# Kernel optimization log

Measured on AMD Instinct MI355X. Metric: run time of the kernel, lower is better.

The kernel has to match this reference:

```python
import jax, jax.numpy as jnp
import numpy as np
import math

D_MODEL, Q, V, H = 512, 64, 64, 8
NEG = float(-2**32 + 1)


def setup_inputs() -> dict:
    key = jax.random.key(0)
    ks = jax.random.split(key, 10)
    B, S = 16, 1024
    x = jax.random.normal(ks[0], (B, S, D_MODEL), dtype=jnp.float32)
    padding_mask = jax.random.randint(ks[1], (B, S), 0, 2, dtype=jnp.int32)
    s = 0.02
    wq = jax.random.normal(ks[2], (D_MODEL, Q * H), dtype=jnp.float32) * s
    bq = jnp.zeros((Q * H,), jnp.float32)
    wk = jax.random.normal(ks[3], (D_MODEL, Q * H), dtype=jnp.float32) * s
    bk = jnp.zeros((Q * H,), jnp.float32)
    wv = jax.random.normal(ks[4], (D_MODEL, V * H), dtype=jnp.float32) * s
    bv = jnp.zeros((V * H,), jnp.float32)
    wo = jax.random.normal(ks[5], (V * H, D_MODEL), dtype=jnp.float32) * s
    bo = jnp.zeros((D_MODEL,), jnp.float32)
    return {"x": x, "padding_mask": padding_mask, "wq": wq, "bq": bq,
            "wk": wk, "bk": bk, "wv": wv, "bv": bv, "wo": wo, "bo": bo}


def _heads_major(t, h, d):
    # torch: cat(t.chunk(h, dim=-1), dim=0): (B,S,h*d) -> (h*B,S,d), head-major
    B, S, _ = t.shape
    return t.reshape(B, S, h, d).transpose(2, 0, 1, 3).reshape(h * B, S, d)


def reference(x, padding_mask, wq, bq, wk, bk, wv, bv, wo, bo):
    B, S, _ = x.shape
    Qh = _heads_major(x @ wq + bq, H, Q)          # (h*B, S, Q)
    Kh = _heads_major(x @ wk + bk, H, Q)          # (h*B, S, Q)
    Vh = _heads_major(x @ wv + bv, H, V)          # (h*B, S, V)
    score = jnp.einsum('nsq,ntq->nst', Qh, Kh) / math.sqrt(Q)  # (h*B,S,S)
    raw_score = score
    # padding mask flattened BATCH-major (B*h), applied to HEAD-major score
    # -- this index mismatch is faithful to the original torch code.
    pm = jnp.broadcast_to(padding_mask[:, None, None, :], (B, H, S, S))
    pm = pm.reshape(B * H, S, S)
    score = jnp.where(pm == 0, NEG, score)
    attn = jnp.einsum('nst,ntv->nsv', jax.nn.softmax(score, axis=-1), Vh)
    # torch: cat(attn.chunk(h, dim=0), dim=-1): (h*B,S,V) -> (B,S,h*V)
    heads = attn.reshape(H, B, S, V).transpose(1, 2, 0, 3).reshape(B, S, H * V)
    out = heads @ wo + bo                          # (B, S, d_model)
    return out, raw_score
```

## Files before the change

kernel.cpp:

```cpp
#include <hip/hip_runtime.h>
#include <hip/hip_bf16.h>

typedef __attribute__((ext_vector_type(8))) short short8;
typedef __attribute__((ext_vector_type(4))) short short4v;
typedef __attribute__((ext_vector_type(4))) float floatx4;

#define NEGVAL (-4294967296.0f)

__device__ __forceinline__ short f2bf(float f) {
    union { float f; unsigned u; } v; v.f = f;
    unsigned r = v.u + 0x7fffu + ((v.u >> 16) & 1u);
    return (short)(r >> 16);
}

__global__ __launch_bounds__(256) void qkv_kernel(
    const float* __restrict__ x,
    const float* __restrict__ wq, const float* __restrict__ bq,
    const float* __restrict__ wk, const float* __restrict__ bk,
    const float* __restrict__ wv, const float* __restrict__ bv,
    short* __restrict__ qws, short* __restrict__ kws, short* __restrict__ vws)
{
    __shared__ __align__(16) short lA[128 * 72];
    __shared__ __align__(16) short lB[128 * 72];

    const int tid  = threadIdx.x;
    const int wave = tid >> 6, lane = tid & 63;
    const int g = lane >> 4, l16 = lane & 15;
    const int m0 = blockIdx.x * 128;
    const int c0 = blockIdx.y * 128;
    const int wsel = c0 >> 9;
    const int cmat = c0 & 511;
    const float* W    = (wsel == 0) ? wq : (wsel == 1) ? wk : wv;
    const float* bias = (wsel == 0) ? bq : (wsel == 1) ? bk : bv;
    short* dst        = (wsel == 0) ? qws : (wsel == 1) ? kws : vws;

    floatx4 acc[4][4];
    #pragma unroll
    for (int i = 0; i < 4; i++)
        #pragma unroll
        for (int j = 0; j < 4; j++) acc[i][j] = (floatx4){0.f, 0.f, 0.f, 0.f};

    const int wm = (wave & 1) * 64, wn = (wave >> 1) * 64;

    for (int k0 = 0; k0 < 512; k0 += 32) {
        #pragma unroll
        for (int it = 0; it < 4; ++it) {
            int u = tid + (it << 8);
            int row = u >> 3, cs = (u & 7) * 4;
            const float4 a = *(const float4*)&x[(size_t)(m0 + row) * 512 + k0 + cs];
            short4v s4;
            s4[0] = f2bf(a.x); s4[1] = f2bf(a.y); s4[2] = f2bf(a.z); s4[3] = f2bf(a.w);
            *(short4v*)&lA[row * 72 + cs] = s4;
        }
        #pragma unroll
        for (int it = 0; it < 4; ++it) {
            int u = tid + (it << 8);
            int d = u >> 5, cs = (u & 31) * 4;
            const float4 b = *(const float4*)&W[(size_t)(k0 + d) * 512 + cmat + cs];
            lB[(cs + 0) * 72 + d] = f2bf(b.x);
            lB[(cs + 1) * 72 + d] = f2bf(b.y);
            lB[(cs + 2) * 72 + d] = f2bf(b.z);
            lB[(cs + 3) * 72 + d] = f2bf(b.w);
        }
        __syncthreads();

        short8 af[4], bf[4];
        #pragma unroll
        for (int i = 0; i < 4; i++)
            af[i] = *(short8*)&lA[(wm + i * 16 + l16) * 72 + (g << 3)];
        #pragma unroll
        for (int j = 0; j < 4; j++)
            bf[j] = *(short8*)&lB[(wn + j * 16 + l16) * 72 + (g << 3)];
        #pragma unroll
        for (int i = 0; i < 4; i++)
            #pragma unroll
            for (int j = 0; j < 4; j++)
                acc[i][j] = __builtin_amdgcn_mfma_f32_16x16x32_bf16(af[i], bf[j], acc[i][j], 0, 0, 0);
        __syncthreads();
    }

    #pragma unroll
    for (int j = 0; j < 4; j++) {
        int cb = cmat + wn + j * 16 + l16;
        float bv_ = bias[cb];
        int h = cb >> 6, qd = cb & 63;
        #pragma unroll
        for (int i = 0; i < 4; i++) {
            #pragma unroll
            for (int r = 0; r < 4; r++) {
                int m = m0 + wm + i * 16 + (g << 2) + r;
                int b = m >> 10, s = m & 1023;
                float v = acc[i][j][r] + bv_;
                dst[(((size_t)((h << 4) + b) << 10) + s) * 64 + qd] = f2bf(v);
            }
        }
    }
}

__global__ __launch_bounds__(256) void attn_kernel(
    const short* __restrict__ qws, const short* __restrict__ kws,
    const short* __restrict__ vws, const int* __restrict__ pm,
    float* __restrict__ raw, short* __restrict__ attnws)
{
    __shared__ __align__(16) short lK[64 * 72];
    __shared__ __align__(16) short lVt[64 * 72];
    __shared__ __align__(16) short lP[4][16 * 72];
    __shared__ float lMask[1024];

    const int tid  = threadIdx.x;
    const int wave = tid >> 6, lane = tid & 63;
    const int g = lane >> 4, l16 = lane & 15;
    const int bx = blockIdx.x;
    const int n  = blockIdx.y;
    const int mb = n >> 3;

    for (int i = tid; i < 1024; i += 256) lMask[i] = (float)pm[(mb << 10) + i];

    const int srow = (bx << 6) + (wave << 4) + l16;
    const size_t qbase = (((size_t)n << 10) + srow) * 64;
    short8 qf0 = *(const short8*)&qws[qbase + (g << 3)];
    short8 qf1 = *(const short8*)&qws[qbase + 32 + (g << 3)];

    float m_r[4], l_r[4];
    floatx4 Of[4];
    #pragma unroll
    for (int r = 0; r < 4; r++) { m_r[r] = -INFINITY; l_r[r] = 0.f; }
    #pragma unroll
    for (int v = 0; v < 4; v++) Of[v] = (floatx4){0.f, 0.f, 0.f, 0.f};

    float* rawn = raw + ((size_t)n << 20);
    const int rowbase = (bx << 6) + (wave << 4) + (g << 2);

    for (int c = 0; c < 16; ++c) {
        const int tc = c << 6;
        #pragma unroll
        for (int it = 0; it < 2; ++it) {
            int u = tid + (it << 8);
            int trow = u >> 3, seg = (u & 7) << 3;
            const size_t gaddr = (((size_t)n << 10) + tc + trow) * 64 + seg;
            *(uint4*)&lK[trow * 72 + seg] = *(const uint4*)&kws[gaddr];
            union { uint4 u4; short s8[8]; } vv;
            vv.u4 = *(const uint4*)&vws[gaddr];
            #pragma unroll
            for (int j = 0; j < 8; j++) lVt[(seg + j) * 72 + trow] = vv.s8[j];
        }
        __syncthreads();

        floatx4 sc[4];
        #pragma unroll
        for (int nt = 0; nt < 4; ++nt) {
            floatx4 a = (floatx4){0.f, 0.f, 0.f, 0.f};
            short8 b0 = *(short8*)&lK[(nt * 16 + l16) * 72 + (g << 3)];
            short8 b1 = *(short8*)&lK[(nt * 16 + l16) * 72 + 32 + (g << 3)];
            a = __builtin_amdgcn_mfma_f32_16x16x32_bf16(qf0, b0, a, 0, 0, 0);
            a = __builtin_amdgcn_mfma_f32_16x16x32_bf16(qf1, b1, a, 0, 0, 0);
            sc[nt] = a;
        }

        float p[4][4];
        float cmax[4] = {-INFINITY, -INFINITY, -INFINITY, -INFINITY};
        #pragma unroll
        for (int nt = 0; nt < 4; ++nt) {
            int col = tc + nt * 16 + l16;
            float mk = lMask[col];
            #pragma unroll
            for (int r = 0; r < 4; r++) {
                float v = sc[nt][r] * 0.125f;
                __builtin_nontemporal_store(v, &rawn[((size_t)(rowbase + r) << 10) + col]);
                float mv = (mk != 0.f) ? v : NEGVAL;
                p[nt][r] = mv;
                cmax[r] = fmaxf(cmax[r], mv);
            }
        }
        #pragma unroll
        for (int off = 1; off < 16; off <<= 1) {
            #pragma unroll
            for (int r = 0; r < 4; r++) cmax[r] = fmaxf(cmax[r], __shfl_xor(cmax[r], off));
        }
        float alpha[4], rs[4];
        #pragma unroll
        for (int r = 0; r < 4; r++) {
            float mn = fmaxf(m_r[r], cmax[r]);
            alpha[r] = __expf(m_r[r] - mn);
            m_r[r] = mn;
            rs[r] = 0.f;
        }
        #pragma unroll
        for (int nt = 0; nt < 4; ++nt) {
            #pragma unroll
            for (int r = 0; r < 4; r++) {
                float e = __expf(p[nt][r] - m_r[r]);
                p[nt][r] = e;
                rs[r] += e;
            }
        }
        #pragma unroll
        for (int off = 1; off < 16; off <<= 1) {
            #pragma unroll
            for (int r = 0; r < 4; r++) rs[r] += __shfl_xor(rs[r], off);
        }
        #pragma unroll
        for (int r = 0; r < 4; r++) l_r[r] = l_r[r] * alpha[r] + rs[r];
        #pragma unroll
        for (int v = 0; v < 4; v++)
            #pragma unroll
            for (int r = 0; r < 4; r++) Of[v][r] *= alpha[r];

        #pragma unroll
        for (int nt = 0; nt < 4; ++nt)
            #pragma unroll
            for (int r = 0; r < 4; r++)
                lP[wave][((g << 2) + r) * 72 + nt * 16 + l16] = f2bf(p[nt][r]);
        __syncthreads();

        #pragma unroll
        for (int ks = 0; ks < 2; ++ks) {
            short8 pa = *(short8*)&lP[wave][l16 * 72 + ks * 32 + (g << 3)];
            #pragma unroll
            for (int v = 0; v < 4; v++) {
                short8 vb = *(short8*)&lVt[(v * 16 + l16) * 72 + ks * 32 + (g << 3)];
                Of[v] = __builtin_amdgcn_mfma_f32_16x16x32_bf16(pa, vb, Of[v], 0, 0, 0);
            }
        }
        __syncthreads();
    }

    const int h = n >> 4, b = n & 15;
    #pragma unroll
    for (int r = 0; r < 4; r++) {
        int s = (bx << 6) + (wave << 4) + (g << 2) + r;
        float inv = 1.f / l_r[r];
        size_t base = ((size_t)((b << 10) + s)) * 512 + (h << 6);
        #pragma unroll
        for (int v = 0; v < 4; v++)
            attnws[base + v * 16 + l16] = f2bf(Of[v][r] * inv);
    }
}

__global__ __launch_bounds__(256) void outproj_kernel(
    const short* __restrict__ attnws, const float* __restrict__ wo,
    const float* __restrict__ bo, float* __restrict__ out)
{
    __shared__ __align__(16) short lA[128 * 72];
    __shared__ __align__(16) short lB[128 * 72];

    const int tid  = threadIdx.x;
    const int wave = tid >> 6, lane = tid & 63;
    const int g = lane >> 4, l16 = lane & 15;
    const int m0 = blockIdx.x * 128;
    const int c0 = blockIdx.y * 128;

    floatx4 acc[4][4];
    #pragma unroll
    for (int i = 0; i < 4; i++)
        #pragma unroll
        for (int j = 0; j < 4; j++) acc[i][j] = (floatx4){0.f, 0.f, 0.f, 0.f};

    const int wm = (wave & 1) * 64, wn = (wave >> 1) * 64;

    for (int k0 = 0; k0 < 512; k0 += 32) {
        #pragma unroll
        for (int it = 0; it < 2; ++it) {
            int u = tid + (it << 8);
            int row = u >> 2, seg = (u & 3) << 3;
            *(uint4*)&lA[row * 72 + seg] =
                *(const uint4*)&attnws[(size_t)(m0 + row) * 512 + k0 + seg];
        }
        #pragma unroll
        for (int it = 0; it < 4; ++it) {
            int u = tid + (it << 8);
            int d = u >> 5, cs = (u & 31) * 4;
            const float4 b = *(const float4*)&wo[(size_t)(k0 + d) * 512 + c0 + cs];
            lB[(cs + 0) * 72 + d] = f2bf(b.x);
            lB[(cs + 1) * 72 + d] = f2bf(b.y);
            lB[(cs + 2) * 72 + d] = f2bf(b.z);
            lB[(cs + 3) * 72 + d] = f2bf(b.w);
        }
        __syncthreads();

        short8 af[4], bf[4];
        #pragma unroll
        for (int i = 0; i < 4; i++)
            af[i] = *(short8*)&lA[(wm + i * 16 + l16) * 72 + (g << 3)];
        #pragma unroll
        for (int j = 0; j < 4; j++)
            bf[j] = *(short8*)&lB[(wn + j * 16 + l16) * 72 + (g << 3)];
        #pragma unroll
        for (int i = 0; i < 4; i++)
            #pragma unroll
            for (int j = 0; j < 4; j++)
                acc[i][j] = __builtin_amdgcn_mfma_f32_16x16x32_bf16(af[i], bf[j], acc[i][j], 0, 0, 0);
        __syncthreads();
    }

    #pragma unroll
    for (int j = 0; j < 4; j++) {
        int cg = c0 + wn + j * 16 + l16;
        float bb = bo[cg];
        #pragma unroll
        for (int i = 0; i < 4; i++) {
            #pragma unroll
            for (int r = 0; r < 4; r++) {
                int m = m0 + wm + i * 16 + (g << 2) + r;
                out[(size_t)m * 512 + cg] = acc[i][j][r] + bb;
            }
        }
    }
}

extern "C" void kernel_launch(void* const* d_in, const int* in_sizes, int n_in,
                              void* d_out, int out_size, void* d_ws, size_t ws_size,
                              hipStream_t stream) {
    const float* x  = (const float*)d_in[0];
    const int*   pm = (const int*)d_in[1];
    const float* wq = (const float*)d_in[2];
    const float* bq = (const float*)d_in[3];
    const float* wk = (const float*)d_in[4];
    const float* bk = (const float*)d_in[5];
    const float* wv = (const float*)d_in[6];
    const float* bv = (const float*)d_in[7];
    const float* wo = (const float*)d_in[8];
    const float* bo = (const float*)d_in[9];

    float* out = (float*)d_out;
    float* raw = out + (size_t)16 * 1024 * 512;

    short* qws    = (short*)d_ws;
    short* kws    = qws + (size_t)128 * 1024 * 64;
    short* vws    = kws + (size_t)128 * 1024 * 64;
    short* attnws = vws + (size_t)128 * 1024 * 64;

    qkv_kernel<<<dim3(128, 12), 256, 0, stream>>>(x, wq, bq, wk, bk, wv, bv, qws, kws, vws);
    attn_kernel<<<dim3(16, 128), 256, 0, stream>>>(qws, kws, vws, pm, raw, attnws);
    outproj_kernel<<<dim3(128, 4), 256, 0, stream>>>(attnws, wo, bo, out);
}
```

Baseline: 817.9 us.

## Pre-convert inputs to bf16, stage tiles via global_load_lds with XOR swizzle, transpose V

Adds separate kernels that convert x to bf16 and convert plus transpose the weight matrices to bf16, so the GEMM kernels no longer convert in the inner loop. The GEMM and attention tile loads now go directly from global memory to LDS through global_load_lds, using an XOR-swizzled layout in place of padding. The QKV kernel writes V already transposed, so the attention kernel no longer transposes it through LDS, and one barrier before the PV step is removed. The cost is two extra kernel launches and extra workspace traffic. The workspace is reused, with x stored in the attention-output buffer, which depends on launch order.

```diff
diff --git a/kernel.cpp b/kernel.cpp
--- a/kernel.cpp
+++ b/kernel.cpp
@@ -13,15 +13,66 @@
     return (short)(r >> 16);
 }
 
+__device__ __forceinline__ void load_lds16(const void* g, void* l) {
+    __builtin_amdgcn_global_load_lds(
+        (const __attribute__((address_space(1))) unsigned int*)g,
+        (__attribute__((address_space(3))) unsigned int*)l, 16, 0, 0);
+}
+
+__global__ __launch_bounds__(256) void convx_kernel(
+    const float* __restrict__ x, short* __restrict__ xbf)
+{
+    size_t i = ((size_t)blockIdx.x * 256 + threadIdx.x) << 3;
+    float4 a = *(const float4*)&x[i];
+    float4 b = *(const float4*)&x[i + 4];
+    short8 s;
+    s[0] = f2bf(a.x); s[1] = f2bf(a.y); s[2] = f2bf(a.z); s[3] = f2bf(a.w);
+    s[4] = f2bf(b.x); s[5] = f2bf(b.y); s[6] = f2bf(b.z); s[7] = f2bf(b.w);
+    *(short8*)&xbf[i] = s;
+}
+
+__global__ __launch_bounds__(256) void convw_kernel(
+    const float* __restrict__ wq, const float* __restrict__ wk,
+    const float* __restrict__ wv, const float* __restrict__ wo,
+    short* __restrict__ wt, short* __restrict__ wot)
+{
+    __shared__ __align__(16) short t[64 * 72];
+    const int tid  = threadIdx.x;
+    const int mat  = blockIdx.x >> 6;
+    const int tile = blockIdx.x & 63;
+    const int tn = (tile >> 3) << 6, tk = (tile & 7) << 6;
+    const float* W = (mat == 0) ? wq : (mat == 1) ? wk : (mat == 2) ? wv : wo;
+    short* dst = (mat < 3) ? (wt + ((size_t)mat << 18)) : wot;
+
+    #pragma unroll
+    for (int it = 0; it < 4; ++it) {
+        int u = tid + (it << 8);
+        int kr = u >> 4, c4 = (u & 15) << 2;
+        const float4 a = *(const float4*)&W[(size_t)(tk + kr) * 512 + tn + c4];
+        short4v s;
+        s[0] = f2bf(a.x); s[1] = f2bf(a.y); s[2] = f2bf(a.z); s[3] = f2bf(a.w);
+        *(short4v*)&t[kr * 72 + c4] = s;
+    }
+    __syncthreads();
+    #pragma unroll
+    for (int it = 0; it < 2; ++it) {
+        int u = tid + (it << 8);
+        int nr = u >> 3, kc = (u & 7) << 3;
+        short8 s;
+        #pragma unroll
+        for (int j = 0; j < 8; ++j) s[j] = t[(kc + j) * 72 + nr];
+        *(short8*)&dst[(size_t)(tn + nr) * 512 + tk + kc] = s;
+    }
+}
+
 __global__ __launch_bounds__(256) void qkv_kernel(
-    const float* __restrict__ x,
-    const float* __restrict__ wq, const float* __restrict__ bq,
-    const float* __restrict__ wk, const float* __restrict__ bk,
-    const float* __restrict__ wv, const float* __restrict__ bv,
+    const short* __restrict__ xbf, const short* __restrict__ wt,
+    const float* __restrict__ bq, const float* __restrict__ bk,
+    const float* __restrict__ bv,
     short* __restrict__ qws, short* __restrict__ kws, short* __restrict__ vws)
 {
-    __shared__ __align__(16) short lA[128 * 72];
-    __shared__ __align__(16) short lB[128 * 72];
+    __shared__ __align__(16) short lA[128 * 32];
+    __shared__ __align__(16) short lB[128 * 32];
 
     const int tid  = threadIdx.x;
     const int wave = tid >> 6, lane = tid & 63;
@@ -30,9 +81,7 @@
     const int c0 = blockIdx.y * 128;
     const int wsel = c0 >> 9;
     const int cmat = c0 & 511;
-    const float* W    = (wsel == 0) ? wq : (wsel == 1) ? wk : wv;
     const float* bias = (wsel == 0) ? bq : (wsel == 1) ? bk : bv;
-    short* dst        = (wsel == 0) ? qws : (wsel == 1) ? kws : vws;
 
     floatx4 acc[4][4];
     #pragma unroll
@@ -41,57 +90,75 @@
         for (int j = 0; j < 4; j++) acc[i][j] = (floatx4){0.f, 0.f, 0.f, 0.f};
 
     const int wm = (wave & 1) * 64, wn = (wave >> 1) * 64;
+    const int lrow = lane >> 2, lch = lane & 3;
+    const int stg = wave << 5;
 
     for (int k0 = 0; k0 < 512; k0 += 32) {
         #pragma unroll
-        for (int it = 0; it < 4; ++it) {
-            int u = tid + (it << 8);
-            int row = u >> 3, cs = (u & 7) * 4;
-            const float4 a = *(const float4*)&x[(size_t)(m0 + row) * 512 + k0 + cs];
-            short4v s4;
-            s4[0] = f2bf(a.x); s4[1] = f2bf(a.y); s4[2] = f2bf(a.z); s4[3] = f2bf(a.w);
-            *(short4v*)&lA[row * 72 + cs] = s4;
-        }
-        #pragma unroll
-        for (int it = 0; it < 4; ++it) {
-            int u = tid + (it << 8);
-            int d = u >> 5, cs = (u & 31) * 4;
-            const float4 b = *(const float4*)&W[(size_t)(k0 + d) * 512 + cmat + cs];
-            lB[(cs + 0) * 72 + d] = f2bf(b.x);
-            lB[(cs + 1) * 72 + d] = f2bf(b.y);
-            lB[(cs + 2) * 72 + d] = f2bf(b.z);
-            lB[(cs + 3) * 72 + d] = f2bf(b.w);
-        }
-        __syncthreads();
-
-        short8 af[4], bf[4];
+        for (int i = 0; i < 2; ++i) {
+            int r = stg + (i << 4) + lrow;
+            load_lds16(&xbf[(size_t)(m0 + r) * 512 + k0 + ((lch ^ ((r >> 1) & 3)) << 3)],
+                       &lA[(stg + (i << 4)) * 32]);
+        }
+        #pragma unroll
+        for (int i = 0; i < 2; ++i) {
+            int r = stg + (i << 4) + lrow;
+            load_lds16(&wt[((size_t)wsel << 18) + (size_t)(cmat + r) * 512 + k0 +
+                           ((lch ^ ((r >> 1) & 3)) << 3)],
+                       &lB[(stg + (i << 4)) * 32]);
+        }
+        __syncthreads();
+
+        short8 af[4], bfr[4];
+        #pragma unroll
+        for (int i = 0; i < 4; i++) {
+            int row = wm + i * 16 + l16;
+            af[i] = *(short8*)&lA[row * 32 + (((g << 3)) ^ ((((row) >> 1) & 3) << 3))];
+        }
+        #pragma unroll
+        for (int j = 0; j < 4; j++) {
+            int row = wn + j * 16 + l16;
+            bfr[j] = *(short8*)&lB[row * 32 + (((g << 3)) ^ ((((row) >> 1) & 3) << 3))];
+        }
         #pragma unroll
         for (int i = 0; i < 4; i++)
-            af[i] = *(short8*)&lA[(wm + i * 16 + l16) * 72 + (g << 3)];
-        #pragma unroll
-        for (int j = 0; j < 4; j++)
-            bf[j] = *(short8*)&lB[(wn + j * 16 + l16) * 72 + (g << 3)];
-        #pragma unroll
-        for (int i = 0; i < 4; i++)
             #pragma unroll
             for (int j = 0; j < 4; j++)
-                acc[i][j] = __builtin_amdgcn_mfma_f32_16x16x32_bf16(af[i], bf[j], acc[i][j], 0, 0, 0);
-        __syncthreads();
-    }
-
-    #pragma unroll
-    for (int j = 0; j < 4; j++) {
-        int cb = cmat + wn + j * 16 + l16;
-        float bv_ = bias[cb];
-        int h = cb >> 6, qd = cb & 63;
-        #pragma unroll
-        for (int i = 0; i < 4; i++) {
-            #pragma unroll
-            for (int r = 0; r < 4; r++) {
-                int m = m0 + wm + i * 16 + (g << 2) + r;
+                acc[i][j] = __builtin_amdgcn_mfma_f32_16x16x32_bf16(af[i], bfr[j], acc[i][j], 0, 0, 0);
+        __syncthreads();
+    }
+
+    if (wsel < 2) {
+        short* dst = wsel ? kws : qws;
+        #pragma unroll
+        for (int j = 0; j < 4; j++) {
+            int cb = cmat + wn + j * 16 + l16;
+            float bv_ = bias[cb];
+            int h = cb >> 6, qd = cb & 63;
+            #pragma unroll
+            for (int i = 0; i < 4; i++) {
+                #pragma unroll
+                for (int r = 0; r < 4; r++) {
+                    int m = m0 + wm + i * 16 + (g << 2) + r;
+                    int b = m >> 10, s = m & 1023;
+                    dst[(((size_t)((h << 4) + b) << 10) + s) * 64 + qd] = f2bf(acc[i][j][r] + bv_);
+                }
+            }
+        }
+    } else {
+        #pragma unroll
+        for (int j = 0; j < 4; j++) {
+            int cb = cmat + wn + j * 16 + l16;
+            float bv_ = bias[cb];
+            int h = cb >> 6, qd = cb & 63;
+            #pragma unroll
+            for (int i = 0; i < 4; i++) {
+                int m = m0 + wm + i * 16 + (g << 2);
                 int b = m >> 10, s = m & 1023;
-                float v = acc[i][j][r] + bv_;
-                dst[(((size_t)((h << 4) + b) << 10) + s) * 64 + qd] = f2bf(v);
+                short4v sv;
+                #pragma unroll
+                for (int r = 0; r < 4; r++) sv[r] = f2bf(acc[i][j][r] + bv_);
+                *(short4v*)&vws[(((size_t)((h << 4) + b) << 6) + qd) * 1024 + s] = sv;
             }
         }
     }
@@ -102,8 +169,8 @@
     const short* __restrict__ vws, const int* __restrict__ pm,
     float* __restrict__ raw, short* __restrict__ attnws)
 {
-    __shared__ __align__(16) short lK[64 * 72];
-    __shared__ __align__(16) short lVt[64 * 72];
+    __shared__ __align__(16) short lK[64 * 64];
+    __shared__ __align__(16) short lVt[64 * 64];
     __shared__ __align__(16) short lP[4][16 * 72];
     __shared__ float lMask[1024];
 
@@ -130,28 +197,33 @@
 
     float* rawn = raw + ((size_t)n << 20);
     const int rowbase = (bx << 6) + (wave << 4) + (g << 2);
+    const int lrow = lane >> 3, lch = lane & 7;
+    const int stg = wave << 4;
 
     for (int c = 0; c < 16; ++c) {
         const int tc = c << 6;
         #pragma unroll
-        for (int it = 0; it < 2; ++it) {
-            int u = tid + (it << 8);
-            int trow = u >> 3, seg = (u & 7) << 3;
-            const size_t gaddr = (((size_t)n << 10) + tc + trow) * 64 + seg;
-            *(uint4*)&lK[trow * 72 + seg] = *(const uint4*)&kws[gaddr];
-            union { uint4 u4; short s8[8]; } vv;
-            vv.u4 = *(const uint4*)&vws[gaddr];
-            #pragma unroll
-            for (int j = 0; j < 8; j++) lVt[(seg + j) * 72 + trow] = vv.s8[j];
+        for (int i = 0; i < 2; ++i) {
+            int r = stg + (i << 3) + lrow;
+            load_lds16(&kws[(((size_t)n << 10) + tc + r) * 64 + ((lch ^ (r & 7)) << 3)],
+                       &lK[(stg + (i << 3)) * 64]);
+        }
+        #pragma unroll
+        for (int i = 0; i < 2; ++i) {
+            int r = stg + (i << 3) + lrow;
+            load_lds16(&vws[(((size_t)n << 6) + r) * 1024 + tc + ((lch ^ (r & 7)) << 3)],
+                       &lVt[(stg + (i << 3)) * 64]);
         }
         __syncthreads();
 
         floatx4 sc[4];
         #pragma unroll
         for (int nt = 0; nt < 4; ++nt) {
+            int rr = nt * 16 + l16;
+            int sw = (rr & 7) << 3;
             floatx4 a = (floatx4){0.f, 0.f, 0.f, 0.f};
-            short8 b0 = *(short8*)&lK[(nt * 16 + l16) * 72 + (g << 3)];
-            short8 b1 = *(short8*)&lK[(nt * 16 + l16) * 72 + 32 + (g << 3)];
+            short8 b0 = *(short8*)&lK[rr * 64 + ((g << 3) ^ sw)];
+            short8 b1 = *(short8*)&lK[rr * 64 + ((32 + (g << 3)) ^ sw)];
             a = __builtin_amdgcn_mfma_f32_16x16x32_bf16(qf0, b0, a, 0, 0, 0);
             a = __builtin_amdgcn_mfma_f32_16x16x32_bf16(qf1, b1, a, 0, 0, 0);
             sc[nt] = a;
@@ -211,14 +283,14 @@
             #pragma unroll
             for (int r = 0; r < 4; r++)
                 lP[wave][((g << 2) + r) * 72 + nt * 16 + l16] = f2bf(p[nt][r]);
-        __syncthreads();
 
         #pragma unroll
         for (int ks = 0; ks < 2; ++ks) {
             short8 pa = *(short8*)&lP[wave][l16 * 72 + ks * 32 + (g << 3)];
             #pragma unroll
             for (int v = 0; v < 4; v++) {
-                short8 vb = *(short8*)&lVt[(v * 16 + l16) * 72 + ks * 32 + (g << 3)];
+                int vr = v * 16 + l16;
+                short8 vb = *(short8*)&lVt[vr * 64 + ((ks * 32 + (g << 3)) ^ ((vr & 7) << 3))];
                 Of[v] = __builtin_amdgcn_mfma_f32_16x16x32_bf16(pa, vb, Of[v], 0, 0, 0);
             }
         }
@@ -238,11 +310,11 @@
 }
 
 __global__ __launch_bounds__(256) void outproj_kernel(
-    const short* __restrict__ attnws, const float* __restrict__ wo,
+    const short* __restrict__ attnws, const short* __restrict__ wot,
     const float* __restrict__ bo, float* __restrict__ out)
 {
-    __shared__ __align__(16) short lA[128 * 72];
-    __shared__ __align__(16) short lB[128 * 72];
+    __shared__ __align__(16) short lA[128 * 32];
+    __shared__ __align__(16) short lB[128 * 32];
 
     const int tid  = threadIdx.x;
     const int wave = tid >> 6, lane = tid & 63;
@@ -257,39 +329,40 @@
         for (int j = 0; j < 4; j++) acc[i][j] = (floatx4){0.f, 0.f, 0.f, 0.f};
 
     const int wm = (wave & 1) * 64, wn = (wave >> 1) * 64;
+    const int lrow = lane >> 2, lch = lane & 3;
+    const int stg = wave << 5;
 
     for (int k0 = 0; k0 < 512; k0 += 32) {
         #pragma unroll
-        for (int it = 0; it < 2; ++it) {
-            int u = tid + (it << 8);
-            int row = u >> 2, seg = (u & 3) << 3;
-            *(uint4*)&lA[row * 72 + seg] =
-                *(const uint4*)&attnws[(size_t)(m0 + row) * 512 + k0 + seg];
-        }
-        #pragma unroll
-        for (int it = 0; it < 4; ++it) {
-            int u = tid + (it << 8);
-            int d = u >> 5, cs = (u & 31) * 4;
-            const float4 b = *(const float4*)&wo[(size_t)(k0 + d) * 512 + c0 + cs];
-            lB[(cs + 0) * 72 + d] = f2bf(b.x);
-            lB[(cs + 1) * 72 + d] = f2bf(b.y);
-            lB[(cs + 2) * 72 + d] = f2bf(b.z);
-            lB[(cs + 3) * 72 + d] = f2bf(b.w);
-        }
-        __syncthreads();
-
-        short8 af[4], bf[4];
+        for (int i = 0; i < 2; ++i) {
+            int r = stg + (i << 4) + lrow;
+            load_lds16(&attnws[(size_t)(m0 + r) * 512 + k0 + ((lch ^ ((r >> 1) & 3)) << 3)],
+                       &lA[(stg + (i << 4)) * 32]);
+        }
+        #pragma unroll
+        for (int i = 0; i < 2; ++i) {
+            int r = stg + (i << 4) + lrow;
+            load_lds16(&wot[(size_t)(c0 + r) * 512 + k0 + ((lch ^ ((r >> 1) & 3)) << 3)],
+                       &lB[(stg + (i << 4)) * 32]);
+        }
+        __syncthreads();
+
+        short8 af[4], bfr[4];
+        #pragma unroll
+        for (int i = 0; i < 4; i++) {
+            int row = wm + i * 16 + l16;
+            af[i] = *(short8*)&lA[row * 32 + ((g << 3) ^ (((row >> 1) & 3) << 3))];
+        }
+        #pragma unroll
+        for (int j = 0; j < 4; j++) {
+            int row = wn + j * 16 + l16;
+            bfr[j] = *(short8*)&lB[row * 32 + ((g << 3) ^ (((row >> 1) & 3) << 3))];
+        }
         #pragma unroll
         for (int i = 0; i < 4; i++)
-            af[i] = *(short8*)&lA[(wm + i * 16 + l16) * 72 + (g << 3)];
-        #pragma unroll
-        for (int j = 0; j < 4; j++)
-            bf[j] = *(short8*)&lB[(wn + j * 16 + l16) * 72 + (g << 3)];
-        #pragma unroll
-        for (int i = 0; i < 4; i++)
             #pragma unroll
             for (int j = 0; j < 4; j++)
-                acc[i][j] = __builtin_amdgcn_mfma_f32_16x16x32_bf16(af[i], bf[j], acc[i][j], 0, 0, 0);
+                acc[i][j] = __builtin_amdgcn_mfma_f32_16x16x32_bf16(af[i], bfr[j], acc[i][j], 0, 0, 0);
         __syncthreads();
     }
 
@@ -329,8 +402,13 @@
     short* kws    = qws + (size_t)128 * 1024 * 64;
     short* vws    = kws + (size_t)128 * 1024 * 64;
     short* attnws = vws + (size_t)128 * 1024 * 64;
-
-    qkv_kernel<<<dim3(128, 12), 256, 0, stream>>>(x, wq, bq, wk, bk, wv, bv, qws, kws, vws);
+    short* xbf    = attnws;
+    short* wt     = attnws + (size_t)128 * 1024 * 64;
+    short* wot    = wt + (size_t)3 * 512 * 512;
+
+    convx_kernel<<<4096, 256, 0, stream>>>(x, xbf);
+    convw_kernel<<<256, 256, 0, stream>>>(wq, wk, wv, wo, wt, wot);
+    qkv_kernel<<<dim3(128, 12), 256, 0, stream>>>(xbf, wt, bq, bk, bv, qws, kws, vws);
     attn_kernel<<<dim3(16, 128), 256, 0, stream>>>(qws, kws, vws, pm, raw, attnws);
-    outproj_kernel<<<dim3(128, 4), 256, 0, stream>>>(attnws, wo, bo, out);
-}
+    outproj_kernel<<<dim3(128, 4), 256, 0, stream>>>(attnws, wot, bo, out);
+}
```

After: 737.7 us. -9.8%, faster.
